# Performance work log

Measured on AMD Instinct MI355X. Metric: run time of the kernel, lower is better.

## Reference

```python
import jax, jax.numpy as jnp
import numpy as np

B, S, D, H = 2, 2048, 2048, 16
HD = D // H  # head_dim = 128


def setup_inputs() -> dict:
    key = jax.random.key(0)
    ks = jax.random.split(key, 5)
    scale = 1.0 / np.sqrt(D)
    return {
        "x": jax.random.normal(ks[0], (B, S, D), dtype=jnp.float32),
        "wq": jax.random.normal(ks[1], (D, D), dtype=jnp.float32) * scale,
        "wk": jax.random.normal(ks[2], (D, D), dtype=jnp.float32) * scale,
        "wv": jax.random.normal(ks[3], (D, D), dtype=jnp.float32) * scale,
        "wo": jax.random.normal(ks[4], (D, D), dtype=jnp.float32) * scale,
        "bo": jnp.zeros((D,), dtype=jnp.float32),
    }


def reference(x, wq, wk, wv, wo, bo):
    b, s, _ = x.shape
    # torch Linear: y = x @ W.T ; then view(b,s,H,HD) and transpose to (b,H,s,HD)
    q = (x @ wq.T).reshape(b, s, H, HD).transpose(0, 2, 1, 3)
    k = (x @ wk.T).reshape(b, s, H, HD).transpose(0, 2, 1, 3)
    v = (x @ wv.T).reshape(b, s, H, HD).transpose(0, 2, 1, 3)
    scores = jnp.einsum("bhqd,bhkd->bhqk", q, k)
    causal = jnp.triu(jnp.ones((s, s), dtype=bool), k=1)  # True above diagonal
    scores = jnp.where(causal[None, None], -jnp.inf, scores)
    attn = jax.nn.softmax(scores / np.sqrt(HD), axis=-1)
    # dropout p=0.0 -> identity
    ctx = jnp.einsum("bhqk,bhkd->bhqd", attn, v)
    ctx = ctx.transpose(0, 2, 1, 3).reshape(b, s, D)
    return ctx @ wo.T + bo
```

## Files before the change

kernel.cpp:

```cpp
#include <hip/hip_runtime.h>
#include <math.h>

typedef __bf16 bf16_t;
typedef __bf16 bf16x8 __attribute__((ext_vector_type(8)));
typedef float f32x4 __attribute__((ext_vector_type(4)));

__device__ __forceinline__ void gload_lds16(const bf16_t* g, bf16_t* l) {
    __builtin_amdgcn_global_load_lds((const __attribute__((address_space(1))) void*)g,
                                     (__attribute__((address_space(3))) void*)l, 16, 0, 0);
}

__global__ __launch_bounds__(256) void cvt_f32_to_bf16(const float* __restrict__ in,
                                                       bf16_t* __restrict__ out, int n8) {
    int i = blockIdx.x * 256 + threadIdx.x;
    if (i >= n8) return;
    const float4* p = (const float4*)in + (size_t)i * 2;
    float4 a = p[0], b = p[1];
    union { bf16_t h[8]; uint4 u; } pk;
    pk.h[0] = (bf16_t)a.x; pk.h[1] = (bf16_t)a.y; pk.h[2] = (bf16_t)a.z; pk.h[3] = (bf16_t)a.w;
    pk.h[4] = (bf16_t)b.x; pk.h[5] = (bf16_t)b.y; pk.h[6] = (bf16_t)b.z; pk.h[7] = (bf16_t)b.w;
    ((uint4*)out)[i] = pk.u;
}

template <typename OutT>
__device__ __forceinline__ void gemm_core(const bf16_t* __restrict__ A,
                                          const bf16_t* __restrict__ Bm,
                                          const float* __restrict__ bias,
                                          OutT* __restrict__ C, int M, int N, int K) {
    __shared__ __align__(16) bf16_t As[2][128 * 32];
    __shared__ __align__(16) bf16_t Bs[2][128 * 32];
    const int tid = threadIdx.x;
    const int l = tid & 63, w = tid >> 6;
    const int l16 = l & 15, lg = l >> 4;
    const int wm = w >> 1, wn = w & 1;
    const int m0 = blockIdx.x * 128, n0 = blockIdx.y * 128;

    f32x4 acc[4][4] = {};

    const int r0 = tid >> 2, r1 = (tid + 256) >> 2, kc = tid & 3;

    auto stageG = [&](int k0, int buf) {
        gload_lds16(A  + (size_t)(m0 + r0) * K + k0 + kc * 8, &As[buf][(w * 64) * 8]);
        gload_lds16(Bm + (size_t)(n0 + r0) * K + k0 + kc * 8, &Bs[buf][(w * 64) * 8]);
        gload_lds16(A  + (size_t)(m0 + r1) * K + k0 + kc * 8, &As[buf][(w * 64 + 256) * 8]);
        gload_lds16(Bm + (size_t)(n0 + r1) * K + k0 + kc * 8, &Bs[buf][(w * 64 + 256) * 8]);
    };

    int cur = 0;
    stageG(0, 0);
    const int nt = K / 32;
    for (int t = 0; t < nt; ++t) {
        __syncthreads();
        if (t + 1 < nt) stageG((t + 1) * 32, cur ^ 1);
        bf16x8 af[4], bfr[4];
#pragma unroll
        for (int i = 0; i < 4; ++i) {
            af[i]  = *(const bf16x8*)&As[cur][(wm * 64 + i * 16 + l16) * 32 + lg * 8];
            bfr[i] = *(const bf16x8*)&Bs[cur][(wn * 64 + i * 16 + l16) * 32 + lg * 8];
        }
#pragma unroll
        for (int mf = 0; mf < 4; ++mf)
#pragma unroll
            for (int nf = 0; nf < 4; ++nf)
                acc[mf][nf] = __builtin_amdgcn_mfma_f32_16x16x32_bf16(af[mf], bfr[nf], acc[mf][nf], 0, 0, 0);
        cur ^= 1;
    }
#pragma unroll
    for (int mf = 0; mf < 4; ++mf) {
#pragma unroll
        for (int nf = 0; nf < 4; ++nf) {
            int col = n0 + wn * 64 + nf * 16 + l16;
            float bv = bias ? bias[col] : 0.f;
#pragma unroll
            for (int r = 0; r < 4; ++r) {
                int row = m0 + wm * 64 + mf * 16 + lg * 4 + r;
                C[(size_t)row * N + col] = (OutT)(acc[mf][nf][r] + bv);
            }
        }
    }
}

__global__ __launch_bounds__(256) void gemm_qkv(const bf16_t* __restrict__ A,
                                                const bf16_t* __restrict__ W0,
                                                const bf16_t* __restrict__ W1,
                                                const bf16_t* __restrict__ W2,
                                                bf16_t* __restrict__ O0, bf16_t* __restrict__ O1,
                                                bf16_t* __restrict__ O2, int M, int N, int K) {
    const bf16_t* Bm = (blockIdx.z == 0) ? W0 : (blockIdx.z == 1) ? W1 : W2;
    bf16_t* C = (blockIdx.z == 0) ? O0 : (blockIdx.z == 1) ? O1 : O2;
    gemm_core<bf16_t>(A, Bm, nullptr, C, M, N, K);
}

__global__ __launch_bounds__(256) void gemm_bias_f32(const bf16_t* __restrict__ A,
                                                     const bf16_t* __restrict__ Bm,
                                                     const float* __restrict__ bias,
                                                     float* __restrict__ C, int M, int N, int K) {
    gemm_core<float>(A, Bm, bias, C, M, N, K);
}

__global__ __launch_bounds__(256) void transpose_v(const bf16_t* __restrict__ V,
                                                   bf16_t* __restrict__ Vt, int S, int H, int Bn) {
    __shared__ bf16_t t[64][72];
    const int s0 = blockIdx.x * 64, d0 = blockIdx.y * 64, b = blockIdx.z;
    const int D = H * 128;
    const int tid = threadIdx.x;
#pragma unroll
    for (int j = 0; j < 2; ++j) {
        int chunk = tid + j * 256;
        int r = chunk >> 3, c8 = chunk & 7;
        *(uint4*)&t[r][c8 * 8] = *(const uint4*)(V + (size_t)(b * S + s0 + r) * D + d0 + c8 * 8);
    }
    __syncthreads();
#pragma unroll
    for (int j = 0; j < 2; ++j) {
        int chunk = tid + j * 256;
        int rr = chunk >> 3, cc = chunk & 7;
        union { bf16_t h[8]; uint4 u; } pk;
#pragma unroll
        for (int u = 0; u < 8; ++u) pk.h[u] = t[cc * 8 + u][rr];
        int dg = d0 + rr;
        size_t idx = ((size_t)(b * H + (dg >> 7)) * 128 + (dg & 127)) * S + s0 + cc * 8;
        *(uint4*)&Vt[idx] = pk.u;
    }
}

__global__ __launch_bounds__(512) void attn_fwd(const bf16_t* __restrict__ Q,
                                                const bf16_t* __restrict__ Kk,
                                                const bf16_t* __restrict__ Vt,
                                                bf16_t* __restrict__ Ctx, int S, int H) {
    const int D = H * 128;
    const int p = blockIdx.x;
    const int bh = blockIdx.y;
    const int b = bh >> 4, h = bh & 15;
    const int tid = threadIdx.x;
    const int w = tid >> 6, l = tid & 63;
    const int l16 = l & 15, lg = l >> 4;

    __shared__ __align__(16) bf16_t ks[2][64 * 128];
    __shared__ __align__(16) bf16_t vs[2][64 * 128];
    __shared__ __align__(16) bf16_t ps[8][16 * 64];

    const float scale = 0.08838834764831845f;
    const f32x4 zero4 = {0.f, 0.f, 0.f, 0.f};

    auto stage = [&](int k0, int buf) {
#pragma unroll
        for (int j = 0; j < 2; ++j) {
            int c = tid + j * 512;
            int r = c >> 4;
            int c8 = (c & 15) ^ (r & 7);
            gload_lds16(Kk + (size_t)(b * S + k0 + r) * D + h * 128 + c8 * 8,
                        &ks[buf][(w * 64 + j * 512) * 8]);
            int dd = c >> 3;
            int k8 = (c & 7) ^ (dd & 7);
            gload_lds16(Vt + ((size_t)bh * 128 + dd) * S + k0 + k8 * 8,
                        &vs[buf][(w * 64 + j * 512) * 8]);
        }
    };

    for (int job = 0; job < 2; ++job) {
        const int qt = job ? (15 - p) : p;
        const int q0 = qt * 128;
        const int nkt = 2 * qt + 2;
        const int rmin = q0 + w * 16, rmax = rmin + 15;

        bf16x8 qf[4];
        {
            const bf16_t* qp = Q + (size_t)(b * S + rmin + l16) * D + h * 128 + lg * 8;
#pragma unroll
            for (int d4 = 0; d4 < 4; ++d4) qf[d4] = *(const bf16x8*)(qp + d4 * 32);
        }
        f32x4 ctx[8];
#pragma unroll
        for (int f = 0; f < 8; ++f) ctx[f] = zero4;
        float mrun[4] = {-INFINITY, -INFINITY, -INFINITY, -INFINITY};
        float lrun[4] = {0.f, 0.f, 0.f, 0.f};

        __syncthreads();
        stage(0, 0);
        int cur = 0;
        for (int kt = 0; kt < nkt; ++kt) {
            __syncthreads();
            if (kt + 1 < nkt) stage((kt + 1) * 64, cur ^ 1);
            const int k0 = kt * 64;
            if (k0 <= rmax) {
                f32x4 sacc[4];
#pragma unroll
                for (int kc = 0; kc < 4; ++kc) sacc[kc] = zero4;
#pragma unroll
                for (int kc = 0; kc < 4; ++kc) {
                    const int krow = kc * 16 + l16;
#pragma unroll
                    for (int d4 = 0; d4 < 4; ++d4) {
                        bf16x8 kf = *(const bf16x8*)&ks[cur][(krow * 16 + ((d4 * 4 + lg) ^ (krow & 7))) * 8];
                        sacc[kc] = __builtin_amdgcn_mfma_f32_16x16x32_bf16(qf[d4], kf, sacc[kc], 0, 0, 0);
                    }
                }
                float sv[4][4];
                const bool needmask = (k0 + 63 > rmin);
#pragma unroll
                for (int kc = 0; kc < 4; ++kc)
#pragma unroll
                    for (int r = 0; r < 4; ++r) {
                        float s = sacc[kc][r] * scale;
                        if (needmask && (k0 + kc * 16 + l16) > (rmin + lg * 4 + r)) s = -INFINITY;
                        sv[kc][r] = s;
                    }
                float alpha[4];
#pragma unroll
                for (int r = 0; r < 4; ++r) {
                    float mx = fmaxf(fmaxf(sv[0][r], sv[1][r]), fmaxf(sv[2][r], sv[3][r]));
#pragma unroll
                    for (int off = 1; off < 16; off <<= 1) mx = fmaxf(mx, __shfl_xor(mx, off));
                    float mnew = fmaxf(mrun[r], mx);
                    alpha[r] = (mrun[r] == -INFINITY) ? 0.f : __expf(mrun[r] - mnew);
                    float psum = 0.f;
#pragma unroll
                    for (int kc = 0; kc < 4; ++kc) {
                        float pe = __expf(sv[kc][r] - mnew);
                        sv[kc][r] = pe;
                        psum += pe;
                    }
#pragma unroll
                    for (int off = 1; off < 16; off <<= 1) psum += __shfl_xor(psum, off);
                    lrun[r] = lrun[r] * alpha[r] + psum;
                    mrun[r] = mnew;
                }
#pragma unroll
                for (int f = 0; f < 8; ++f) {
                    ctx[f][0] *= alpha[0]; ctx[f][1] *= alpha[1];
                    ctx[f][2] *= alpha[2]; ctx[f][3] *= alpha[3];
                }
#pragma unroll
                for (int r = 0; r < 4; ++r) {
                    int prow = lg * 4 + r;
#pragma unroll
                    for (int kc = 0; kc < 4; ++kc)
                        ps[w][prow * 64 + ((kc * 16 + l16) ^ ((prow & 7) << 3))] = (bf16_t)sv[kc][r];
                }
#pragma unroll
                for (int t = 0; t < 2; ++t) {
                    bf16x8 pa = *(const bf16x8*)&ps[w][l16 * 64 + ((t * 32 + lg * 8) ^ ((l16 & 7) << 3))];
#pragma unroll
                    for (int f = 0; f < 8; ++f) {
                        bf16x8 vb = *(const bf16x8*)&vs[cur][((f * 16 + l16) * 8 + ((t * 4 + lg) ^ (l16 & 7))) * 8];
                        ctx[f] = __builtin_amdgcn_mfma_f32_16x16x32_bf16(pa, vb, ctx[f], 0, 0, 0);
                    }
                }
            }
            cur ^= 1;
        }
        float invl[4];
#pragma unroll
        for (int r = 0; r < 4; ++r) invl[r] = 1.f / lrun[r];
#pragma unroll
        for (int f = 0; f < 8; ++f)
#pragma unroll
            for (int r = 0; r < 4; ++r) {
                int qrow = rmin + lg * 4 + r;
                Ctx[(size_t)(b * S + qrow) * D + h * 128 + f * 16 + l16] = (bf16_t)(ctx[f][r] * invl[r]);
            }
    }
}

extern "C" void kernel_launch(void* const* d_in, const int* in_sizes, int n_in,
                              void* d_out, int out_size, void* d_ws, size_t ws_size,
                              hipStream_t stream) {
    const int B = 2, S = 2048, D = 2048, H = 16;
    const int M = B * S;
    const float* x  = (const float*)d_in[0];
    const float* wq = (const float*)d_in[1];
    const float* wk = (const float*)d_in[2];
    const float* wv = (const float*)d_in[3];
    const float* wo = (const float*)d_in[4];
    const float* bo = (const float*)d_in[5];
    float* out = (float*)d_out;

    char* ws = (char*)d_ws;
    const size_t MB = 1024 * 1024;
    if (ws_size < 128 * MB) return;
    bf16_t* xb  = (bf16_t*)(ws);
    bf16_t* wqb = (bf16_t*)(ws + 16 * MB);
    bf16_t* wkb = (bf16_t*)(ws + 24 * MB);
    bf16_t* wvb = (bf16_t*)(ws + 32 * MB);
    bf16_t* wob = (bf16_t*)(ws + 40 * MB);
    bf16_t* qb  = (bf16_t*)(ws + 48 * MB);
    bf16_t* kb  = (bf16_t*)(ws + 64 * MB);
    bf16_t* vb  = (bf16_t*)(ws + 80 * MB);
    bf16_t* vtb = (bf16_t*)(ws + 96 * MB);
    bf16_t* cxb = (bf16_t*)(ws + 112 * MB);

    cvt_f32_to_bf16<<<M * D / 8 / 256, 256, 0, stream>>>(x, xb, M * D / 8);
    cvt_f32_to_bf16<<<D * D / 8 / 256, 256, 0, stream>>>(wq, wqb, D * D / 8);
    cvt_f32_to_bf16<<<D * D / 8 / 256, 256, 0, stream>>>(wk, wkb, D * D / 8);
    cvt_f32_to_bf16<<<D * D / 8 / 256, 256, 0, stream>>>(wv, wvb, D * D / 8);
    cvt_f32_to_bf16<<<D * D / 8 / 256, 256, 0, stream>>>(wo, wob, D * D / 8);

    gemm_qkv<<<dim3(M / 128, D / 128, 3), 256, 0, stream>>>(xb, wqb, wkb, wvb, qb, kb, vb, M, D, D);
    transpose_v<<<dim3(S / 64, D / 64, B), 256, 0, stream>>>(vb, vtb, S, H, B);
    attn_fwd<<<dim3(8, B * H), 512, 0, stream>>>(qb, kb, vtb, cxb, S, H);
    gemm_bias_f32<<<dim3(M / 128, D / 128), 256, 0, stream>>>(cxb, wob, bo, out, M, D, D);
}
```

Baseline: 309.3 us.

## Rework GEMM core into 256x128x64 tiles with swizzled LDS and XCD-aware block remap

Restructures the shared GEMM core to use 512-thread blocks computing 256x128 output tiles with a K-step of 64, XOR-swizzled LDS layout to avoid bank conflicts, and a four-phase inner loop that interleaves prefetch of the next tile with MFMA work under explicit barriers and priority hints. Block indices are remapped so consecutive workgroups dispatched to the same XCD cover neighbouring tiles, improving L2 reuse. This aims to raise MFMA utilisation and cut global/LDS traffic per FLOP in the QKV and output projections, at the cost of much larger LDS use (96KB) and more complex hand-scheduled synchronisation that could limit occupancy.

```diff
diff --git a/kernel.cpp b/kernel.cpp
--- a/kernel.cpp
+++ b/kernel.cpp
@@ -26,76 +26,119 @@
 __device__ __forceinline__ void gemm_core(const bf16_t* __restrict__ A,
                                           const bf16_t* __restrict__ Bm,
                                           const float* __restrict__ bias,
-                                          OutT* __restrict__ C, int M, int N, int K) {
-    __shared__ __align__(16) bf16_t As[2][128 * 32];
-    __shared__ __align__(16) bf16_t Bs[2][128 * 32];
+                                          OutT* __restrict__ C, int M, int N, int K,
+                                          int bx, int by) {
+    __shared__ __align__(16) bf16_t As[2][256 * 64];
+    __shared__ __align__(16) bf16_t Bs[2][128 * 64];
     const int tid = threadIdx.x;
-    const int l = tid & 63, w = tid >> 6;
+    const int w = tid >> 6, l = tid & 63;
     const int l16 = l & 15, lg = l >> 4;
-    const int wm = w >> 1, wn = w & 1;
-    const int m0 = blockIdx.x * 128, n0 = blockIdx.y * 128;
+    const int wr = w >> 1, wc = w & 1;
+    const int m0 = bx * 256, n0 = by * 128;
+    const int lsw = l16 & 7;
 
     f32x4 acc[4][4] = {};
 
-    const int r0 = tid >> 2, r1 = (tid + 256) >> 2, kc = tid & 3;
-
-    auto stageG = [&](int k0, int buf) {
-        gload_lds16(A  + (size_t)(m0 + r0) * K + k0 + kc * 8, &As[buf][(w * 64) * 8]);
-        gload_lds16(Bm + (size_t)(n0 + r0) * K + k0 + kc * 8, &Bs[buf][(w * 64) * 8]);
-        gload_lds16(A  + (size_t)(m0 + r1) * K + k0 + kc * 8, &As[buf][(w * 64 + 256) * 8]);
-        gload_lds16(Bm + (size_t)(n0 + r1) * K + k0 + kc * 8, &Bs[buf][(w * 64 + 256) * 8]);
+    auto stageA = [&](int k0, int buf, int half) {
+#pragma unroll
+        for (int j = 0; j < 2; ++j) {
+            int c = tid + (half * 2 + j) * 512;
+            int row = c >> 3;
+            int kc = (c & 7) ^ (row & 7);
+            gload_lds16(A + (size_t)(m0 + row) * K + k0 + kc * 8,
+                        &As[buf][(w * 64 + (half * 2 + j) * 512) * 8]);
+        }
     };
-
-    int cur = 0;
-    stageG(0, 0);
-    const int nt = K / 32;
+    auto stageB = [&](int k0, int buf) {
+#pragma unroll
+        for (int j = 0; j < 2; ++j) {
+            int c = tid + j * 512;
+            int row = c >> 3;
+            int kc = (c & 7) ^ (row & 7);
+            gload_lds16(Bm + (size_t)(n0 + row) * K + k0 + kc * 8,
+                        &Bs[buf][(w * 64 + j * 512) * 8]);
+        }
+    };
+
+    stageA(0, 0, 0); stageA(0, 0, 1); stageB(0, 0);
+    asm volatile("s_waitcnt vmcnt(0)" ::: "memory");
+    __builtin_amdgcn_s_barrier();
+
+    const int nt = K / 64;
     for (int t = 0; t < nt; ++t) {
-        __syncthreads();
-        if (t + 1 < nt) stageG((t + 1) * 32, cur ^ 1);
-        bf16x8 af[4], bfr[4];
-#pragma unroll
-        for (int i = 0; i < 4; ++i) {
-            af[i]  = *(const bf16x8*)&As[cur][(wm * 64 + i * 16 + l16) * 32 + lg * 8];
-            bfr[i] = *(const bf16x8*)&Bs[cur][(wn * 64 + i * 16 + l16) * 32 + lg * 8];
-        }
-#pragma unroll
-        for (int mf = 0; mf < 4; ++mf)
-#pragma unroll
-            for (int nf = 0; nf < 4; ++nf)
-                acc[mf][nf] = __builtin_amdgcn_mfma_f32_16x16x32_bf16(af[mf], bfr[nf], acc[mf][nf], 0, 0, 0);
-        cur ^= 1;
+        const int cur = t & 1;
+        const int k1 = (t + 1) * 64;
+        const bool pf = (t + 1 < nt);
+#pragma unroll
+        for (int p = 0; p < 4; ++p) {
+            const int mh = p >> 1, nh = p & 1;
+            bf16x8 af[2][2], bfr[2][2];
+#pragma unroll
+            for (int i = 0; i < 2; ++i)
+#pragma unroll
+                for (int ks = 0; ks < 2; ++ks) {
+                    int arow = wr * 64 + (mh * 2 + i) * 16 + l16;
+                    af[i][ks] = *(const bf16x8*)&As[cur][arow * 64 + (((ks << 2) | lg) ^ lsw) * 8];
+                    int brow = wc * 64 + (nh * 2 + i) * 16 + l16;
+                    bfr[i][ks] = *(const bf16x8*)&Bs[cur][brow * 64 + (((ks << 2) | lg) ^ lsw) * 8];
+                }
+            if (pf) {
+                if (p == 0) { stageA(k1, cur ^ 1, 0); stageA(k1, cur ^ 1, 1); }
+                else if (p == 1) { stageB(k1, cur ^ 1); }
+            }
+            __builtin_amdgcn_s_barrier();
+            asm volatile("s_waitcnt lgkmcnt(0)" ::: "memory");
+            __builtin_amdgcn_sched_barrier(0);
+            __builtin_amdgcn_s_setprio(1);
+#pragma unroll
+            for (int ks = 0; ks < 2; ++ks)
+#pragma unroll
+                for (int i = 0; i < 2; ++i)
+#pragma unroll
+                    for (int jn = 0; jn < 2; ++jn)
+                        acc[mh * 2 + i][nh * 2 + jn] = __builtin_amdgcn_mfma_f32_16x16x32_bf16(
+                            af[i][ks], bfr[jn][ks], acc[mh * 2 + i][nh * 2 + jn], 0, 0, 0);
+            __builtin_amdgcn_s_setprio(0);
+            if (p == 3) asm volatile("s_waitcnt vmcnt(0)" ::: "memory");
+            __builtin_amdgcn_s_barrier();
+        }
     }
 #pragma unroll
-    for (int mf = 0; mf < 4; ++mf) {
+    for (int mf = 0; mf < 4; ++mf)
 #pragma unroll
         for (int nf = 0; nf < 4; ++nf) {
-            int col = n0 + wn * 64 + nf * 16 + l16;
+            int col = n0 + wc * 64 + nf * 16 + l16;
             float bv = bias ? bias[col] : 0.f;
 #pragma unroll
             for (int r = 0; r < 4; ++r) {
-                int row = m0 + wm * 64 + mf * 16 + lg * 4 + r;
+                int row = m0 + wr * 64 + mf * 16 + lg * 4 + r;
                 C[(size_t)row * N + col] = (OutT)(acc[mf][nf][r] + bv);
             }
         }
-    }
-}
-
-__global__ __launch_bounds__(256) void gemm_qkv(const bf16_t* __restrict__ A,
-                                                const bf16_t* __restrict__ W0,
-                                                const bf16_t* __restrict__ W1,
-                                                const bf16_t* __restrict__ W2,
-                                                bf16_t* __restrict__ O0, bf16_t* __restrict__ O1,
-                                                bf16_t* __restrict__ O2, int M, int N, int K) {
-    const bf16_t* Bm = (blockIdx.z == 0) ? W0 : (blockIdx.z == 1) ? W1 : W2;
-    bf16_t* C = (blockIdx.z == 0) ? O0 : (blockIdx.z == 1) ? O1 : O2;
-    gemm_core<bf16_t>(A, Bm, nullptr, C, M, N, K);
-}
-
-__global__ __launch_bounds__(256) void gemm_bias_f32(const bf16_t* __restrict__ A,
-                                                     const bf16_t* __restrict__ Bm,
-                                                     const float* __restrict__ bias,
-                                                     float* __restrict__ C, int M, int N, int K) {
-    gemm_core<float>(A, Bm, bias, C, M, N, K);
+}
+
+__global__ __launch_bounds__(512, 2) void gemm_qkv(const bf16_t* __restrict__ A,
+                                                   const bf16_t* __restrict__ W0,
+                                                   const bf16_t* __restrict__ W1,
+                                                   const bf16_t* __restrict__ W2,
+                                                   bf16_t* __restrict__ O0, bf16_t* __restrict__ O1,
+                                                   bf16_t* __restrict__ O2, int M, int N, int K) {
+    int flat = blockIdx.x + 16 * (blockIdx.y + 16 * blockIdx.z);
+    int idx = (flat & 7) * 96 + (flat >> 3);
+    int bx = idx & 15, by = (idx >> 4) & 15, bz = idx >> 8;
+    const bf16_t* Bm = (bz == 0) ? W0 : (bz == 1) ? W1 : W2;
+    bf16_t* Cp = (bz == 0) ? O0 : (bz == 1) ? O1 : O2;
+    gemm_core<bf16_t>(A, Bm, nullptr, Cp, M, N, K, bx, by);
+}
+
+__global__ __launch_bounds__(512, 2) void gemm_bias_f32(const bf16_t* __restrict__ A,
+                                                        const bf16_t* __restrict__ Bm,
+                                                        const float* __restrict__ bias,
+                                                        float* __restrict__ C, int M, int N, int K) {
+    int flat = blockIdx.x + 16 * blockIdx.y;
+    int idx = (flat & 7) * 32 + (flat >> 3);
+    int bx = idx & 15, by = idx >> 4;
+    gemm_core<float>(A, Bm, bias, C, M, N, K, bx, by);
 }
 
 __global__ __launch_bounds__(256) void transpose_v(const bf16_t* __restrict__ V,
@@ -296,8 +339,8 @@
     cvt_f32_to_bf16<<<D * D / 8 / 256, 256, 0, stream>>>(wv, wvb, D * D / 8);
     cvt_f32_to_bf16<<<D * D / 8 / 256, 256, 0, stream>>>(wo, wob, D * D / 8);
 
-    gemm_qkv<<<dim3(M / 128, D / 128, 3), 256, 0, stream>>>(xb, wqb, wkb, wvb, qb, kb, vb, M, D, D);
+    gemm_qkv<<<dim3(16, 16, 3), 512, 0, stream>>>(xb, wqb, wkb, wvb, qb, kb, vb, M, D, D);
     transpose_v<<<dim3(S / 64, D / 64, B), 256, 0, stream>>>(vb, vtb, S, H, B);
     attn_fwd<<<dim3(8, B * H), 512, 0, stream>>>(qb, kb, vtb, cxb, S, H);
-    gemm_bias_f32<<<dim3(M / 128, D / 128), 256, 0, stream>>>(cxb, wob, bo, out, M, D, D);
-}
+    gemm_bias_f32<<<dim3(16, 16), 512, 0, stream>>>(cxb, wob, bo, out, M, D, D);
+}
```

After: 356.7 us. 1.15x slower.
